# Performance work log

Hardware: AMD Instinct MI355X
Metric: run time of the kernel (lower is better)

## Reference

```python
import jax, jax.numpy as jnp
import numpy as np

NUM_KERNELS = 5


def setup_inputs() -> dict:
    key = jax.random.key(0)
    k1, k2 = jax.random.split(key)
    B, D = 4096, 256
    return {
        "s_feat": jax.random.normal(k1, (B, D), dtype=jnp.float32),
        "t_feat": jax.random.normal(k2, (B, D), dtype=jnp.float32),
    }


def _pairwise_sq_dists(feats):
    # Gram-matrix form of sum((x_i - x_j)**2, axis=-1); same math as the
    # broadcasted (x - y)**2 sum, without the [N, N, D] intermediate.
    sq = jnp.sum(feats * feats, axis=-1)  # [N]
    d = sq[:, None] + sq[None, :] - 2.0 * (feats @ feats.T)  # [N, N]
    return jnp.maximum(d, 0.0)


def reference(s_feat, t_feat):
    batch = s_feat.shape[0]
    feats = jnp.concatenate((s_feat, t_feat), axis=0)  # [2B, D]
    distances = _pairwise_sq_dists(feats)  # [2B, 2B]

    # Median-heuristic-style bandwidth (detached in original).
    n = 2 * batch
    bandwidth = float(n * n - n) / jnp.sum(jax.lax.stop_gradient(distances))
    bandwidth = bandwidth / (2 ** (NUM_KERNELS // 2))
    gammas = [bandwidth * (2 ** i) for i in range(NUM_KERNELS)]

    # Multi-gamma Gaussian kernel average (fixed small loop over kernels).
    kern = sum(jnp.exp(-distances * g) for g in gammas) / NUM_KERNELS

    s2s = kern[:batch, :batch]
    t2t = kern[batch:, batch:]
    s2t = kern[:batch, batch:]
    disc = jnp.mean(s2s + t2t - 2.0 * s2t)
    return disc
```

## Files before the change

### kernel.cpp

```cpp
#include <hip/hip_runtime.h>
#include <stdint.h>
#include <math.h>

#define BATCH 4096
#define NT    8192
#define FD    256
#define TM    256
#define TN    128
#define BK    32
#define NUMK  5
#define NBLK  1056

typedef __attribute__((ext_vector_type(8))) short bf16x8;
typedef __attribute__((ext_vector_type(4))) float f32x4;

static const size_t WS_FB    = 0;
static const size_t WS_SQ    = (size_t)NT * FD * 2;
static const size_t WS_COL   = WS_SQ + (size_t)NT * 4;
static const size_t WS_SUMSQ = WS_COL + 256 * 4;

__device__ __forceinline__ unsigned short f2bf_rne(float x) {
    unsigned u = __float_as_uint(x);
    unsigned r = (u + 0x7fffu + ((u >> 16) & 1u)) >> 16;
    return (unsigned short)r;
}

__device__ __forceinline__ void async_copy16(void* lds, const void* g) {
    __builtin_amdgcn_global_load_lds(
        (__attribute__((address_space(1))) void*)(void*)(const_cast<void*>(g)),
        (__attribute__((address_space(3))) void*)lds, 16, 0, 0);
}

__global__ void mmd_prep(const float* __restrict__ s_feat,
                         const float* __restrict__ t_feat,
                         unsigned short* __restrict__ fb,
                         float* __restrict__ sq,
                         float* __restrict__ colsum,
                         float* __restrict__ sumsq,
                         float* __restrict__ out) {
    __shared__ float cp[4][FD];
    if (blockIdx.x == 0 && threadIdx.x == 0) atomicExch(out, 0.0f);
    const int w    = threadIdx.x >> 6;
    const int lane = threadIdx.x & 63;
    float c0 = 0.f, c1 = 0.f, c2 = 0.f, c3 = 0.f;
    float wtot = 0.f;
    for (int t = 0; t < 8; ++t) {
        int row = blockIdx.x * 32 + w * 8 + t;
        const float* src = (row < BATCH) ? (s_feat + (size_t)row * FD)
                                         : (t_feat + (size_t)(row - BATCH) * FD);
        float4 v = ((const float4*)src)[lane];
        unsigned int u01 = (unsigned)f2bf_rne(v.x) | ((unsigned)f2bf_rne(v.y) << 16);
        unsigned int u23 = (unsigned)f2bf_rne(v.z) | ((unsigned)f2bf_rne(v.w) << 16);
        ((uint2*)(fb + (size_t)row * FD))[lane] = make_uint2(u01, u23);
        float ss = v.x * v.x + v.y * v.y + v.z * v.z + v.w * v.w;
        for (int off = 32; off; off >>= 1) ss += __shfl_down(ss, off);
        if (lane == 0) { sq[row] = ss; wtot += ss; }
        c0 += v.x; c1 += v.y; c2 += v.z; c3 += v.w;
    }
    if (lane == 0) atomicAdd(sumsq, wtot);
    cp[w][4 * lane + 0] = c0;
    cp[w][4 * lane + 1] = c1;
    cp[w][4 * lane + 2] = c2;
    cp[w][4 * lane + 3] = c3;
    __syncthreads();
    int t = threadIdx.x;
    float s = cp[0][t] + cp[1][t] + cp[2][t] + cp[3][t];
    atomicAdd(&colsum[t], s);
}

__global__ __launch_bounds__(512, 4) void mmd_main(
    const unsigned short* __restrict__ fb,
    const float* __restrict__ sq,
    const float* __restrict__ colsum,
    const float* __restrict__ sumsq,
    float* __restrict__ out) {
    const int bid = blockIdx.x;
    const int swz = (bid & 7) * (NBLK / 8) + (bid >> 3);
    int I = (int)((65.0f - sqrtf(fmaxf(4225.0f - 4.0f * (float)swz, 0.f))) * 0.5f);
    if (I > 31) I = 31;
    while (I > 0 && I * (65 - I) > swz) --I;
    while (I < 31 && (I + 1) * (65 - (I + 1)) <= swz) ++I;
    const int J = 2 * I + (swz - I * (65 - I));
    const bool straddle = ((J >> 1) == I);

    __shared__ __align__(16) unsigned short a_t[3][TM * BK];
    __shared__ __align__(16) unsigned short b_t[3][TN * BK];
    __shared__ float sqa[TM], sqb[TN];
    __shared__ float red[8];

    const int tid  = threadIdx.x;
    const int w    = tid >> 6, lane = tid & 63;
    const int wm2  = w >> 1, wn2 = w & 1;
    const int quad = lane >> 4, m16 = lane & 15;
    const int lrow16 = lane >> 2;
    const int pslot  = lane & 3;

    const size_t rowA0 = (size_t)I * TM;
    const size_t rowB0 = (size_t)J * TN;

    float sqv = 0.f;
    if (tid < TM)                sqv = sq[rowA0 + tid];
    else if (tid < TM + TN)      sqv = sq[rowB0 + (tid - TM)];
    float4 c4 = ((const float4*)colsum)[lane];

#define STAGE(buf, k0_) do {                                                   \
        _Pragma("unroll")                                                      \
        for (int q = 0; q < 2; ++q) {                                          \
            int rr_ = w * 32 + q * 16 + lrow16;                    \
            int gc_ = pslot ^ ((rr_ >> 1) & 3);                                \
            async_copy16(&a_t[buf][(w * 32 + q * 16) * BK],                    \
                         fb + (rowA0 + rr_) * FD + (k0_) + gc_ * 8);           \
        }                                                                      \
        {                                                                      \
            int rr_ = w * 16 + lrow16;                             \
            int gc_ = pslot ^ ((rr_ >> 1) & 3);                                \
            async_copy16(&b_t[buf][(w * 16) * BK],                             \
                         fb + (rowB0 + rr_) * FD + (k0_) + gc_ * 8);           \
        }                                                                      \
    } while (0)

    STAGE(0, 0);
    STAGE(1, BK);
    STAGE(2, 2 * BK);

    float cv = c4.x * c4.x + c4.y * c4.y + c4.z * c4.z + c4.w * c4.w;
    for (int off = 1; off < 64; off <<= 1) cv += __shfl_xor(cv, off);
    const float sumd = 2.0f * (float)NT * sumsq[0] - 2.0f * cv;
    const float n2n  = (float)((long long)NT * NT - NT);
    const float g0   = 0.25f * (n2n / sumd);

    if (tid < TM)                sqa[tid] = sqv;
    else if (tid < TM + TN)      sqb[tid - TM] = sqv;

    const f32x4 fzero = {0.f, 0.f, 0.f, 0.f};
    f32x4 acc[4][4];
#pragma unroll
    for (int a = 0; a < 4; ++a)
#pragma unroll
        for (int b = 0; b < 4; ++b) acc[a][b] = fzero;

    __syncthreads();

#pragma unroll
    for (int st = 0; st < 8; ++st) {
        if (st > 0) {
            if (st >= 3) {
                if (st == 7) asm volatile("s_waitcnt vmcnt(0)" ::: "memory");
                else         asm volatile("s_waitcnt vmcnt(3)" ::: "memory");
            }
            __builtin_amdgcn_s_barrier();
            __builtin_amdgcn_sched_barrier(0);
            if (st <= 5) STAGE((st + 2) % 3, (st + 2) * BK);
        }
        const int cur = st % 3;

        bf16x8 af[4], bf[4];
#pragma unroll
        for (int tm = 0; tm < 4; ++tm) {
            int row = wm2 * 64 + tm * 16 + m16;
            int p = quad ^ ((row >> 1) & 3);
            af[tm] = *(const bf16x8*)&a_t[cur][row * BK + p * 8];
        }
#pragma unroll
        for (int tn = 0; tn < 4; ++tn) {
            int row = wn2 * 64 + tn * 16 + m16;
            int p = quad ^ ((row >> 1) & 3);
            bf[tn] = *(const bf16x8*)&b_t[cur][row * BK + p * 8];
        }
        __builtin_amdgcn_sched_barrier(0);

        __builtin_amdgcn_s_setprio(1);
#pragma unroll
        for (int tm = 0; tm < 4; ++tm)
#pragma unroll
            for (int tn = 0; tn < 4; ++tn)
                acc[tm][tn] = __builtin_amdgcn_mfma_f32_16x16x32_bf16(
                    af[tm], bf[tn], acc[tm][tn], 0, 0, 0);
        __builtin_amdgcn_s_setprio(0);
    }

    float ls[4] = {0.f, 0.f, 0.f, 0.f};
    if (!straddle) {
#pragma unroll
        for (int tm = 0; tm < 4; ++tm) {
            const int i0 = wm2 * 64 + tm * 16 + quad * 4;
            float sqi[4] = {sqa[i0 + 0], sqa[i0 + 1], sqa[i0 + 2], sqa[i0 + 3]};
#pragma unroll
            for (int tn = 0; tn < 4; ++tn) {
                const int j = wn2 * 64 + tn * 16 + m16;
                const float sqj = sqb[j];
#pragma unroll
                for (int rr = 0; rr < 4; ++rr) {
                    float d = fmaf(-2.f, acc[tm][tn][rr], sqi[rr] + sqj);
                    d = fmaxf(d, 0.f);
                    float e1 = __expf(-d * g0);
                    float e2 = e1 * e1, e4 = e2 * e2, e8 = e4 * e4, e16 = e8 * e8;
                    ls[rr] += e1 + e2 + e4 + e8 + e16;
                }
            }
        }
    } else {
        const int dOff = (J - 2 * I) * TN;
#pragma unroll
        for (int tm = 0; tm < 4; ++tm) {
            const int i0 = wm2 * 64 + tm * 16 + quad * 4;
            float sqi[4] = {sqa[i0 + 0], sqa[i0 + 1], sqa[i0 + 2], sqa[i0 + 3]};
#pragma unroll
            for (int tn = 0; tn < 4; ++tn) {
                const int j = wn2 * 64 + tn * 16 + m16;
                const float sqj = sqb[j];
                const int jg = j + dOff;
#pragma unroll
                for (int rr = 0; rr < 4; ++rr) {
                    const int ig = i0 + rr;
                    float wf = (jg > ig) ? 2.f : ((jg == ig) ? 1.f : 0.f);
                    float d = fmaf(-2.f, acc[tm][tn][rr], sqi[rr] + sqj);
                    d = fmaxf(d, 0.f);
                    float e1 = __expf(-d * g0);
                    float e2 = e1 * e1, e4 = e2 * e2, e8 = e4 * e4, e16 = e8 * e8;
                    ls[rr] += wf * (e1 + e2 + e4 + e8 + e16);
                }
            }
        }
    }
    float lsum = (ls[0] + ls[1]) + (ls[2] + ls[3]);
    for (int off = 32; off; off >>= 1) lsum += __shfl_down(lsum, off);
    if (lane == 0) red[w] = lsum;
    __syncthreads();
    if (tid == 0) {
        float wgt;
        if (straddle) wgt = 1.f;
        else wgt = ((I < 16) == (J < 32)) ? 2.f : -2.f;
        float scale = wgt * (1.f / NUMK) * (1.f / 16777216.f);
        float tot = ((red[0] + red[1]) + (red[2] + red[3]))
                  + ((red[4] + red[5]) + (red[6] + red[7]));
        atomicAdd(out, tot * scale);
    }
}

extern "C" void kernel_launch(void* const* d_in, const int* in_sizes, int n_in,
                              void* d_out, int out_size, void* d_ws, size_t ws_size,
                              hipStream_t stream) {
    const float* s_feat = (const float*)d_in[0];
    const float* t_feat = (const float*)d_in[1];
    char* ws = (char*)d_ws;
    unsigned short* fb = (unsigned short*)(ws + WS_FB);
    float* sq     = (float*)(ws + WS_SQ);
    float* colsum = (float*)(ws + WS_COL);
    float* sumsq  = (float*)(ws + WS_SUMSQ);
    float* out    = (float*)d_out;

    hipMemsetAsync(ws + WS_COL, 0, 256 * 4 + 4, stream);

    mmd_prep<<<NT / 32, 256, 0, stream>>>(s_feat, t_feat, fb, sq, colsum, sumsq, out);
    mmd_main<<<NBLK, 512, 0, stream>>>(fb, sq, colsum, sumsq, out);
}
```

Measured before the change: 115.0 us.

## Replace atomic column-sum reduction with per-block partials and a gamma kernel

The prep kernel now runs 1024 blocks of 8 rows each and writes per-block column and squared-norm partials instead of doing global atomicAdds. A new single-block kernel reduces those partials, computes the bandwidth gamma and zeroes the output. The main kernel then just reads gamma instead of recomputing it per block, and the memset is gone. The aim is to remove atomic contention and the memset and to give prep more parallelism, at the cost of an extra kernel launch and a serial single-block reduction step.

```diff
diff --git a/kernel.cpp b/kernel.cpp
--- a/kernel.cpp
+++ b/kernel.cpp
@@ -10,14 +10,16 @@
 #define BK    32
 #define NUMK  5
 #define NBLK  1056
+#define PBLK  1024
 
 typedef __attribute__((ext_vector_type(8))) short bf16x8;
 typedef __attribute__((ext_vector_type(4))) float f32x4;
 
 static const size_t WS_FB    = 0;
 static const size_t WS_SQ    = (size_t)NT * FD * 2;
-static const size_t WS_COL   = WS_SQ + (size_t)NT * 4;
-static const size_t WS_SUMSQ = WS_COL + 256 * 4;
+static const size_t WS_PCOL  = WS_SQ + (size_t)NT * 4;
+static const size_t WS_WSUM  = WS_PCOL + (size_t)PBLK * 256 * 4;
+static const size_t WS_GAMMA = WS_WSUM + (size_t)PBLK * 4;
 
 __device__ __forceinline__ unsigned short f2bf_rne(float x) {
     unsigned u = __float_as_uint(x);
@@ -35,17 +37,17 @@
                          const float* __restrict__ t_feat,
                          unsigned short* __restrict__ fb,
                          float* __restrict__ sq,
-                         float* __restrict__ colsum,
-                         float* __restrict__ sumsq,
-                         float* __restrict__ out) {
+                         float* __restrict__ pcol,
+                         float* __restrict__ wsum) {
     __shared__ float cp[4][FD];
-    if (blockIdx.x == 0 && threadIdx.x == 0) atomicExch(out, 0.0f);
+    __shared__ float rw[4];
     const int w    = threadIdx.x >> 6;
     const int lane = threadIdx.x & 63;
     float c0 = 0.f, c1 = 0.f, c2 = 0.f, c3 = 0.f;
     float wtot = 0.f;
-    for (int t = 0; t < 8; ++t) {
-        int row = blockIdx.x * 32 + w * 8 + t;
+#pragma unroll
+    for (int t = 0; t < 2; ++t) {
+        int row = blockIdx.x * 8 + w * 2 + t;
         const float* src = (row < BATCH) ? (s_feat + (size_t)row * FD)
                                          : (t_feat + (size_t)(row - BATCH) * FD);
         float4 v = ((const float4*)src)[lane];
@@ -57,22 +59,62 @@
         if (lane == 0) { sq[row] = ss; wtot += ss; }
         c0 += v.x; c1 += v.y; c2 += v.z; c3 += v.w;
     }
-    if (lane == 0) atomicAdd(sumsq, wtot);
     cp[w][4 * lane + 0] = c0;
     cp[w][4 * lane + 1] = c1;
     cp[w][4 * lane + 2] = c2;
     cp[w][4 * lane + 3] = c3;
+    if (lane == 0) rw[w] = wtot;
     __syncthreads();
     int t = threadIdx.x;
-    float s = cp[0][t] + cp[1][t] + cp[2][t] + cp[3][t];
-    atomicAdd(&colsum[t], s);
+    pcol[(size_t)blockIdx.x * 256 + t] = cp[0][t] + cp[1][t] + cp[2][t] + cp[3][t];
+    if (t == 0) wsum[blockIdx.x] = rw[0] + rw[1] + rw[2] + rw[3];
+}
+
+__global__ void mmd_gamma(const float* __restrict__ pcol,
+                          const float* __restrict__ wsum,
+                          float* __restrict__ gamma,
+                          float* __restrict__ out) {
+    __shared__ float gcol[4][256];
+    __shared__ float redc[4], redw[16];
+    const int tid  = threadIdx.x;
+    const int c    = tid & 255, s = tid >> 8;
+    const int lane = tid & 63;
+    float a0 = 0.f, a1 = 0.f, a2 = 0.f, a3 = 0.f;
+#pragma unroll 4
+    for (int k = 0; k < 256; k += 4) {
+        a0 += pcol[(size_t)(s * 256 + k + 0) * 256 + c];
+        a1 += pcol[(size_t)(s * 256 + k + 1) * 256 + c];
+        a2 += pcol[(size_t)(s * 256 + k + 2) * 256 + c];
+        a3 += pcol[(size_t)(s * 256 + k + 3) * 256 + c];
+    }
+    gcol[s][c] = (a0 + a1) + (a2 + a3);
+    float wv = wsum[tid];
+    for (int off = 32; off; off >>= 1) wv += __shfl_down(wv, off);
+    if (lane == 0) redw[tid >> 6] = wv;
+    __syncthreads();
+    if (tid < 256) {
+        float colv = gcol[0][c] + gcol[1][c] + gcol[2][c] + gcol[3][c];
+        float cv2 = colv * colv;
+        for (int off = 32; off; off >>= 1) cv2 += __shfl_down(cv2, off);
+        if (lane == 0) redc[tid >> 6] = cv2;
+    }
+    __syncthreads();
+    if (tid == 0) {
+        float s2 = (redc[0] + redc[1]) + (redc[2] + redc[3]);
+        float ssq = 0.f;
+#pragma unroll
+        for (int i = 0; i < 16; ++i) ssq += redw[i];
+        float sumd = 2.0f * (float)NT * ssq - 2.0f * s2;
+        float n2n  = (float)((long long)NT * NT - NT);
+        gamma[0]   = 0.25f * (n2n / sumd);
+        out[0]     = 0.f;
+    }
 }
 
 __global__ __launch_bounds__(512, 4) void mmd_main(
     const unsigned short* __restrict__ fb,
     const float* __restrict__ sq,
-    const float* __restrict__ colsum,
-    const float* __restrict__ sumsq,
+    const float* __restrict__ gamma,
     float* __restrict__ out) {
     const int bid = blockIdx.x;
     const int swz = (bid & 7) * (NBLK / 8) + (bid >> 3);
@@ -101,7 +143,7 @@
     float sqv = 0.f;
     if (tid < TM)                sqv = sq[rowA0 + tid];
     else if (tid < TM + TN)      sqv = sq[rowB0 + (tid - TM)];
-    float4 c4 = ((const float4*)colsum)[lane];
+    const float g0 = gamma[0];
 
 #define STAGE(buf, k0_) do {                                                   \
         _Pragma("unroll")                                                      \
@@ -123,12 +165,6 @@
     STAGE(1, BK);
     STAGE(2, 2 * BK);
 
-    float cv = c4.x * c4.x + c4.y * c4.y + c4.z * c4.z + c4.w * c4.w;
-    for (int off = 1; off < 64; off <<= 1) cv += __shfl_xor(cv, off);
-    const float sumd = 2.0f * (float)NT * sumsq[0] - 2.0f * cv;
-    const float n2n  = (float)((long long)NT * NT - NT);
-    const float g0   = 0.25f * (n2n / sumd);
-
     if (tid < TM)                sqa[tid] = sqv;
     else if (tid < TM + TN)      sqb[tid - TM] = sqv;
 
@@ -245,13 +281,13 @@
     const float* t_feat = (const float*)d_in[1];
     char* ws = (char*)d_ws;
     unsigned short* fb = (unsigned short*)(ws + WS_FB);
-    float* sq     = (float*)(ws + WS_SQ);
-    float* colsum = (float*)(ws + WS_COL);
-    float* sumsq  = (float*)(ws + WS_SUMSQ);
-    float* out    = (float*)d_out;
-
-    hipMemsetAsync(ws + WS_COL, 0, 256 * 4 + 4, stream);
-
-    mmd_prep<<<NT / 32, 256, 0, stream>>>(s_feat, t_feat, fb, sq, colsum, sumsq, out);
-    mmd_main<<<NBLK, 512, 0, stream>>>(fb, sq, colsum, sumsq, out);
-}
+    float* sq    = (float*)(ws + WS_SQ);
+    float* pcol  = (float*)(ws + WS_PCOL);
+    float* wsum  = (float*)(ws + WS_WSUM);
+    float* gamma = (float*)(ws + WS_GAMMA);
+    float* out   = (float*)d_out;
+
+    mmd_prep<<<PBLK, 256, 0, stream>>>(s_feat, t_feat, fb, sq, pcol, wsum);
+    mmd_gamma<<<1, 1024, 0, stream>>>(pcol, wsum, gamma, out);
+    mmd_main<<<NBLK, 512, 0, stream>>>(fb, sq, gamma, out);
+}
```

After: 108.1 us. 5.9% less time.
